# Kernel tuning notes

Measured on AMD Instinct MI355X. Metric: run time of the kernel, lower is better.

The kernel has to match this reference:

```python
import jax, jax.numpy as jnp
import numpy as np

EMBED, HEAD, CTX = 1024, 64, 2048

def setup_inputs() -> dict:
    key = jax.random.key(0)
    k1, k2, k3, k4 = jax.random.split(key, 4)
    x = jax.random.normal(k1, (16, 2048, EMBED), dtype=jnp.float32)
    s = EMBED ** -0.5  # torch Linear default init scale-ish
    Wq = jax.random.normal(k2, (EMBED, HEAD), dtype=jnp.float32) * s
    Wk = jax.random.normal(k3, (EMBED, HEAD), dtype=jnp.float32) * s
    Wv = jax.random.normal(k4, (EMBED, HEAD), dtype=jnp.float32) * s
    return {"x": x, "Wq": Wq, "Wk": Wk, "Wv": Wv}

def reference(x, Wq, Wk, Wv):
    # x: [B, S, E] -> q,k,v: [B, S, H]
    q = jnp.einsum('bse,eh->bsh', x, Wq)
    k = jnp.einsum('bse,eh->bsh', x, Wk)
    v = jnp.einsum('bse,eh->bsh', x, Wv)
    scale = k.shape[-1] ** -0.5
    scores = jnp.einsum('bqh,bkh->bqk', q, k) * scale  # [B, S, S]
    S = x.shape[1]
    causal = jnp.tril(jnp.ones((S, S), dtype=bool))
    scores = jnp.where(causal, scores, -jnp.inf)
    attn = jax.nn.softmax(scores, axis=-1)
    return jnp.einsum('bqk,bkh->bqh', attn, v)  # [B, S, H]
```

## Files before the change

### kernel.cpp

```cpp
#include <hip/hip_runtime.h>
#include <math.h>

#define BATCH 16
#define SEQ   2048
#define EMB   1024
#define HD    64
#define NROWS (BATCH*SEQ)

typedef __attribute__((ext_vector_type(8))) short short8;
typedef __attribute__((ext_vector_type(4))) float f32x4;

#define SWZ(byte, row) ((byte) ^ (((row) & 7) << 4))

__device__ __forceinline__ ushort f2bf(float f) {
    union { float f; unsigned u; } c; c.f = f;
    return (ushort)((c.u + 0x7FFF + ((c.u >> 16) & 1)) >> 16);
}

__global__ void k_transpose_w(const float* __restrict__ Wq,
                              const float* __restrict__ Wk,
                              const float* __restrict__ Wv,
                              ushort* __restrict__ wt) {
    int idx  = blockIdx.x * 256 + threadIdx.x;
    int c192 = idx >> 10;
    int e    = idx & 1023;
    const float* W = (c192 < 64) ? Wq : (c192 < 128 ? Wk : Wv);
    wt[idx] = f2bf(W[e * HD + (c192 & 63)]);
}

__global__ __launch_bounds__(256)
void k_qkv_proj(const float* __restrict__ x, const ushort* __restrict__ wt,
                ushort* __restrict__ qkv) {
    __shared__ short8 smem[(8192 + 24576) / 16];
    char* xls = (char*)smem;
    char* wls = (char*)smem + 8192;
    const int t = threadIdx.x;
    const int lane = t & 63, w = t >> 6;
    const int l15 = lane & 15, lg = lane >> 4;
    const int row0 = blockIdx.x * 64;

    f32x4 acc[3][4];
    #pragma unroll
    for (int mi = 0; mi < 3; ++mi)
        #pragma unroll
        for (int n = 0; n < 4; ++n) acc[mi][n] = (f32x4){0.f,0.f,0.f,0.f};

    for (int ch = 0; ch < EMB / 64; ++ch) {
        __syncthreads();
        #pragma unroll
        for (int i = 0; i < 4; ++i) {
            int c = t + i * 256;
            int r = c >> 4, f4 = c & 15;
            float4 v = *(const float4*)&x[(size_t)(row0 + r) * EMB + ch * 64 + f4 * 4];
            ushort4 bv;
            bv.x = f2bf(v.x); bv.y = f2bf(v.y); bv.z = f2bf(v.z); bv.w = f2bf(v.w);
            *(ushort4*)(xls + SWZ(r * 128 + f4 * 8, r)) = bv;
        }
        #pragma unroll
        for (int i = 0; i < 6; ++i) {
            int c = t + i * 256;
            int cr = c >> 3, j = c & 7;
            short8 v = *(const short8*)&wt[(size_t)cr * EMB + ch * 64 + j * 8];
            *(short8*)(wls + SWZ(cr * 128 + j * 16, cr)) = v;
        }
        __syncthreads();
        #pragma unroll
        for (int s = 0; s < 2; ++s) {
            short8 xf[4], wf[3];
            #pragma unroll
            for (int n = 0; n < 4; ++n) {
                int r = n * 16 + l15;
                xf[n] = *(short8*)(xls + SWZ(r * 128 + s * 64 + lg * 16, r));
            }
            #pragma unroll
            for (int mi = 0; mi < 3; ++mi) {
                int cr = w * 48 + mi * 16 + l15;
                wf[mi] = *(short8*)(wls + SWZ(cr * 128 + s * 64 + lg * 16, cr));
            }
            #pragma unroll
            for (int mi = 0; mi < 3; ++mi)
                #pragma unroll
                for (int n = 0; n < 4; ++n)
                    acc[mi][n] = __builtin_amdgcn_mfma_f32_16x16x32_bf16(
                        wf[mi], xf[n], acc[mi][n], 0, 0, 0);
        }
    }
    #pragma unroll
    for (int mi = 0; mi < 3; ++mi) {
        int cg0 = w * 48 + mi * 16 + 4 * lg;
        int m = cg0 >> 6, c = cg0 & 63;
        float sc = (m == 0) ? 0.125f : 1.0f;
        #pragma unroll
        for (int n = 0; n < 4; ++n) {
            int row = row0 + n * 16 + l15;
            ushort4 o;
            o.x = f2bf(acc[mi][n][0] * sc);
            o.y = f2bf(acc[mi][n][1] * sc);
            o.z = f2bf(acc[mi][n][2] * sc);
            o.w = f2bf(acc[mi][n][3] * sc);
            *(ushort4*)&qkv[((size_t)m * NROWS + row) * HD + c] = o;
        }
    }
}

__global__ __launch_bounds__(256)
void k_vt(const ushort* __restrict__ v, ushort* __restrict__ vt) {
    __shared__ short8 sm[64 * 72 / 8];
    ushort* lds = (ushort*)sm;
    const int t = threadIdx.x;
    const int b = blockIdx.x >> 5, k0 = (blockIdx.x & 31) * 64;
    #pragma unroll
    for (int i = 0; i < 2; ++i) {
        int c = t + i * 256;
        int key = c >> 3, j = c & 7;
        short8 d = *(const short8*)&v[((size_t)b * SEQ + k0 + key) * HD + j * 8];
        #pragma unroll
        for (int e = 0; e < 8; ++e) lds[(j * 8 + e) * 72 + key] = (ushort)d[e];
    }
    __syncthreads();
    #pragma unroll
    for (int i = 0; i < 2; ++i) {
        int c = t + i * 256;
        int hd = c >> 3, j = c & 7;
        short8 d = *(short8*)&lds[hd * 72 + j * 8];
        *(short8*)&vt[((size_t)b * HD + hd) * SEQ + k0 + j * 8] = d;
    }
}

__global__ __launch_bounds__(256)
void k_attn(const ushort* __restrict__ q, const ushort* __restrict__ k,
            const ushort* __restrict__ vt, float* __restrict__ out) {
    __shared__ short8 smem[(8192 + 8192 + 8192) / 16];
    char* kls = (char*)smem;
    char* vls = (char*)smem + 8192;
    char* pls = (char*)smem + 16384;
    const int t = threadIdx.x, lane = t & 63, w = t >> 6;
    const int l15 = lane & 15, lg = lane >> 4;
    const int b = blockIdx.x & 15, qt = 31 - (blockIdx.x >> 4);
    const int row0 = qt * 64;
    const int r0w = row0 + w * 16;
    const ushort* qb = q  + (size_t)b * SEQ * HD;
    const ushort* kb = k  + (size_t)b * SEQ * HD;
    const ushort* vb = vt + (size_t)b * HD * SEQ;
    char* pw = pls + w * 2048;

    short8 qf[2];
    #pragma unroll
    for (int s = 0; s < 2; ++s)
        qf[s] = *(const short8*)&qb[(size_t)(r0w + l15) * HD + s * 32 + lg * 8];

    f32x4 oacc[4];
    #pragma unroll
    for (int h = 0; h < 4; ++h) oacc[h] = (f32x4){0.f,0.f,0.f,0.f};
    float m_ = -INFINITY, l_ = 0.f;

    const int nkt = qt + 1;
    for (int kt = 0; kt < nkt; ++kt) {
        const int k0 = kt * 64;
        __syncthreads();
        #pragma unroll
        for (int i = 0; i < 2; ++i) {
            int c = t + i * 256;
            int r = c >> 3, j = c & 7;
            short8 kv = *(const short8*)&kb[(size_t)(k0 + r) * HD + j * 8];
            *(short8*)(kls + SWZ(r * 128 + j * 16, r)) = kv;
            short8 vv = *(const short8*)&vb[(size_t)r * SEQ + k0 + j * 8];
            *(short8*)(vls + SWZ(r * 128 + j * 16, r)) = vv;
        }
        __syncthreads();

        f32x4 sa[4];
        #pragma unroll
        for (int a = 0; a < 4; ++a) sa[a] = (f32x4){0.f,0.f,0.f,0.f};
        #pragma unroll
        for (int s = 0; s < 2; ++s)
            #pragma unroll
            for (int a = 0; a < 4; ++a) {
                int r = a * 16 + l15;
                short8 kf = *(short8*)(kls + SWZ(r * 128 + s * 64 + lg * 16, r));
                sa[a] = __builtin_amdgcn_mfma_f32_16x16x32_bf16(kf, qf[s], sa[a], 0, 0, 0);
            }

        if (kt == nkt - 1) {
            int qrow = r0w + l15;
            #pragma unroll
            for (int a = 0; a < 4; ++a)
                #pragma unroll
                for (int r = 0; r < 4; ++r)
                    if (k0 + a * 16 + 4 * lg + r > qrow) sa[a][r] = -INFINITY;
        }

        float smax = -INFINITY;
        #pragma unroll
        for (int a = 0; a < 4; ++a)
            #pragma unroll
            for (int r = 0; r < 4; ++r) smax = fmaxf(smax, sa[a][r]);
        smax = fmaxf(smax, __shfl_xor(smax, 16));
        smax = fmaxf(smax, __shfl_xor(smax, 32));
        float mn   = fmaxf(m_, smax);
        float corr = __expf(m_ - mn);
        float p[16], ps = 0.f;
        #pragma unroll
        for (int a = 0; a < 4; ++a)
            #pragma unroll
            for (int r = 0; r < 4; ++r) {
                float pv = __expf(sa[a][r] - mn);
                p[a * 4 + r] = pv; ps += pv;
            }
        ps += __shfl_xor(ps, 16);
        ps += __shfl_xor(ps, 32);
        l_ = l_ * corr + ps;
        m_ = mn;
        #pragma unroll
        for (int h = 0; h < 4; ++h) oacc[h] *= corr;

        #pragma unroll
        for (int a = 0; a < 4; ++a) {
            ushort4 pb;
            pb.x = f2bf(p[a * 4 + 0]); pb.y = f2bf(p[a * 4 + 1]);
            pb.z = f2bf(p[a * 4 + 2]); pb.w = f2bf(p[a * 4 + 3]);
            *(ushort4*)(pw + SWZ(l15 * 128 + a * 32 + lg * 8, l15)) = pb;
        }

        #pragma unroll
        for (int c = 0; c < 2; ++c) {
            short8 pf = *(short8*)(pw + SWZ(l15 * 128 + c * 64 + lg * 16, l15));
            #pragma unroll
            for (int h = 0; h < 4; ++h) {
                int r = h * 16 + l15;
                short8 vf = *(short8*)(vls + SWZ(r * 128 + c * 64 + lg * 16, r));
                oacc[h] = __builtin_amdgcn_mfma_f32_16x16x32_bf16(vf, pf, oacc[h], 0, 0, 0);
            }
        }
    }

    float inv = 1.0f / l_;
    #pragma unroll
    for (int h = 0; h < 4; ++h)
        #pragma unroll
        for (int r = 0; r < 4; ++r) {
            int hd = h * 16 + 4 * lg + r;
            out[((size_t)b * SEQ + r0w + l15) * HD + hd] = oacc[h][r] * inv;
        }
}

extern "C" void kernel_launch(void* const* d_in, const int* in_sizes, int n_in,
                              void* d_out, int out_size, void* d_ws, size_t ws_size,
                              hipStream_t stream) {
    const float* x  = (const float*)d_in[0];
    const float* Wq = (const float*)d_in[1];
    const float* Wk = (const float*)d_in[2];
    const float* Wv = (const float*)d_in[3];
    float* out = (float*)d_out;
    ushort* ws = (ushort*)d_ws;
    ushort* wt16  = ws;
    ushort* qkv16 = ws + 192 * 1024;
    ushort* vt16  = qkv16 + (size_t)3 * NROWS * HD;

    k_transpose_w<<<768, 256, 0, stream>>>(Wq, Wk, Wv, wt16);
    k_qkv_proj  <<<NROWS / 64, 256, 0, stream>>>(x, wt16, qkv16);
    k_vt        <<<BATCH * (SEQ / 64), 256, 0, stream>>>(
                    qkv16 + (size_t)2 * NROWS * HD, vt16);
    k_attn      <<<BATCH * (SEQ / 64), 256, 0, stream>>>(
                    qkv16, qkv16 + (size_t)NROWS * HD, vt16, out);
}
```

Measured before the change: 80.55 us.

## Double-buffer projection and attention loads, fuse V transpose, add lazy softmax rescale

```diff
diff --git a/kernel.cpp b/kernel.cpp
--- a/kernel.cpp
+++ b/kernel.cpp
@@ -10,11 +10,18 @@
 typedef __attribute__((ext_vector_type(8))) short short8;
 typedef __attribute__((ext_vector_type(4))) float f32x4;
 
-#define SWZ(byte, row) ((byte) ^ (((row) & 7) << 4))
+#define SWZ(byte, row)   ((byte) ^ (((row) & 7) << 4))
+#define SWZ16(byte, row) ((byte) ^ (((row) & 15) << 4))
 
 __device__ __forceinline__ ushort f2bf(float f) {
     union { float f; unsigned u; } c; c.f = f;
     return (ushort)((c.u + 0x7FFF + ((c.u >> 16) & 1)) >> 16);
+}
+
+__device__ __forceinline__ void gload_lds16(const void* g, void* l) {
+    __builtin_amdgcn_global_load_lds(
+        (const __attribute__((address_space(1))) void*)g,
+        (__attribute__((address_space(3))) void*)l, 16, 0, 0);
 }
 
 __global__ void k_transpose_w(const float* __restrict__ Wq,
@@ -30,12 +37,10 @@
 
 __global__ __launch_bounds__(256)
 void k_qkv_proj(const float* __restrict__ x, const ushort* __restrict__ wt,
-                ushort* __restrict__ qkv) {
-    __shared__ short8 smem[(8192 + 24576) / 16];
-    char* xls = (char*)smem;
-    char* wls = (char*)smem + 8192;
-    const int t = threadIdx.x;
-    const int lane = t & 63, w = t >> 6;
+                ushort* __restrict__ qkv, ushort* __restrict__ vt) {
+    __shared__ short8 smem[65536 / 16];
+    char* base = (char*)smem;
+    const int t = threadIdx.x, lane = t & 63, w = t >> 6;
     const int l15 = lane & 15, lg = lane >> 4;
     const int row0 = blockIdx.x * 64;
 
@@ -43,102 +48,137 @@
     #pragma unroll
     for (int mi = 0; mi < 3; ++mi)
         #pragma unroll
-        for (int n = 0; n < 4; ++n) acc[mi][n] = (f32x4){0.f,0.f,0.f,0.f};
-
-    for (int ch = 0; ch < EMB / 64; ++ch) {
-        __syncthreads();
-        #pragma unroll
-        for (int i = 0; i < 4; ++i) {
-            int c = t + i * 256;
-            int r = c >> 4, f4 = c & 15;
-            float4 v = *(const float4*)&x[(size_t)(row0 + r) * EMB + ch * 64 + f4 * 4];
-            ushort4 bv;
-            bv.x = f2bf(v.x); bv.y = f2bf(v.y); bv.z = f2bf(v.z); bv.w = f2bf(v.w);
-            *(ushort4*)(xls + SWZ(r * 128 + f4 * 8, r)) = bv;
-        }
+        for (int n = 0; n < 4; ++n) acc[mi][n] = (f32x4){0.f, 0.f, 0.f, 0.f};
+
+    float4 xr[2][2];
+
+    auto issue_x = [&](int ch) {
+        #pragma unroll
+        for (int i = 0; i < 2; ++i) {
+            int fidx = t + i * 256;
+            int r = fidx >> 3, j = fidx & 7;
+            const float* src = &x[(size_t)(row0 + r) * EMB + ch * 64 + j * 8];
+            xr[i][0] = *(const float4*)(src);
+            xr[i][1] = *(const float4*)(src + 4);
+        }
+    };
+    auto write_x = [&](int buf) {
+        char* xb = base + buf * 32768;
+        #pragma unroll
+        for (int i = 0; i < 2; ++i) {
+            int fidx = t + i * 256;
+            int r = fidx >> 3, j = fidx & 7;
+            short8 o;
+            o[0] = (short)f2bf(xr[i][0].x); o[1] = (short)f2bf(xr[i][0].y);
+            o[2] = (short)f2bf(xr[i][0].z); o[3] = (short)f2bf(xr[i][0].w);
+            o[4] = (short)f2bf(xr[i][1].x); o[5] = (short)f2bf(xr[i][1].y);
+            o[6] = (short)f2bf(xr[i][1].z); o[7] = (short)f2bf(xr[i][1].w);
+            *(short8*)(xb + SWZ(r * 128 + j * 16, r)) = o;
+        }
+    };
+    auto issue_w = [&](int ch, int buf) {
+        char* wb = base + buf * 32768 + 8192;
         #pragma unroll
         for (int i = 0; i < 6; ++i) {
-            int c = t + i * 256;
-            int cr = c >> 3, j = c & 7;
-            short8 v = *(const short8*)&wt[(size_t)cr * EMB + ch * 64 + j * 8];
-            *(short8*)(wls + SWZ(cr * 128 + j * 16, cr)) = v;
-        }
-        __syncthreads();
+            int r = (w * 6 + i) * 8 + (lane >> 3);
+            int j = (lane & 7) ^ (r & 7);
+            gload_lds16(&wt[(size_t)r * EMB + ch * 64 + j * 8],
+                        wb + (w * 6 + i) * 1024);
+        }
+    };
+    auto compute = [&](int buf) {
+        char* xb = base + buf * 32768;
+        char* wb = base + buf * 32768 + 8192;
         #pragma unroll
         for (int s = 0; s < 2; ++s) {
             short8 xf[4], wf[3];
             #pragma unroll
             for (int n = 0; n < 4; ++n) {
                 int r = n * 16 + l15;
-                xf[n] = *(short8*)(xls + SWZ(r * 128 + s * 64 + lg * 16, r));
+                xf[n] = *(short8*)(xb + SWZ(r * 128 + s * 64 + lg * 16, r));
             }
             #pragma unroll
             for (int mi = 0; mi < 3; ++mi) {
                 int cr = w * 48 + mi * 16 + l15;
-                wf[mi] = *(short8*)(wls + SWZ(cr * 128 + s * 64 + lg * 16, cr));
-            }
-            #pragma unroll
-            for (int mi = 0; mi < 3; ++mi)
+                wf[mi] = *(short8*)(wb + SWZ(cr * 128 + s * 64 + lg * 16, cr));
+            }
+            __builtin_amdgcn_s_setprio(1);
+            #pragma unroll
+            for (int mi = 0; mi < 3; ++mi) {
+                bool vsec = (w * 48 + mi * 16) >= 128;
                 #pragma unroll
                 for (int n = 0; n < 4; ++n)
-                    acc[mi][n] = __builtin_amdgcn_mfma_f32_16x16x32_bf16(
-                        wf[mi], xf[n], acc[mi][n], 0, 0, 0);
-        }
-    }
+                    acc[mi][n] = vsec
+                        ? __builtin_amdgcn_mfma_f32_16x16x32_bf16(xf[n], wf[mi], acc[mi][n], 0, 0, 0)
+                        : __builtin_amdgcn_mfma_f32_16x16x32_bf16(wf[mi], xf[n], acc[mi][n], 0, 0, 0);
+            }
+            __builtin_amdgcn_s_setprio(0);
+        }
+    };
+
+    issue_x(0); issue_w(0, 0); write_x(0);
+    __syncthreads();
+    for (int ch = 0; ch < 16; ++ch) {
+        int cur = ch & 1, nxt = cur ^ 1;
+        if (ch < 15) { issue_w(ch + 1, nxt); issue_x(ch + 1); }
+        compute(cur);
+        if (ch < 15) write_x(nxt);
+        __syncthreads();
+    }
+
+    char* qkb = base;
+    char* vtb = base + 16384;
+    const float qscale = 0.125f * 1.44269504f;
     #pragma unroll
     for (int mi = 0; mi < 3; ++mi) {
-        int cg0 = w * 48 + mi * 16 + 4 * lg;
-        int m = cg0 >> 6, c = cg0 & 63;
-        float sc = (m == 0) ? 0.125f : 1.0f;
+        int cg0 = w * 48 + mi * 16;
+        bool vsec = cg0 >= 128;
         #pragma unroll
         for (int n = 0; n < 4; ++n) {
-            int row = row0 + n * 16 + l15;
             ushort4 o;
-            o.x = f2bf(acc[mi][n][0] * sc);
-            o.y = f2bf(acc[mi][n][1] * sc);
-            o.z = f2bf(acc[mi][n][2] * sc);
-            o.w = f2bf(acc[mi][n][3] * sc);
-            *(ushort4*)&qkv[((size_t)m * NROWS + row) * HD + c] = o;
-        }
-    }
-}
-
-__global__ __launch_bounds__(256)
-void k_vt(const ushort* __restrict__ v, ushort* __restrict__ vt) {
-    __shared__ short8 sm[64 * 72 / 8];
-    ushort* lds = (ushort*)sm;
-    const int t = threadIdx.x;
-    const int b = blockIdx.x >> 5, k0 = (blockIdx.x & 31) * 64;
+            if (!vsec) {
+                float sc = (cg0 < 64) ? qscale : 1.0f;
+                o.x = f2bf(acc[mi][n][0] * sc); o.y = f2bf(acc[mi][n][1] * sc);
+                o.z = f2bf(acc[mi][n][2] * sc); o.w = f2bf(acc[mi][n][3] * sc);
+                int xrow = n * 16 + l15, c = cg0 + lg * 4;
+                *(ushort4*)(qkb + SWZ16(xrow * 256 + c * 2, xrow)) = o;
+            } else {
+                o.x = f2bf(acc[mi][n][0]); o.y = f2bf(acc[mi][n][1]);
+                o.z = f2bf(acc[mi][n][2]); o.w = f2bf(acc[mi][n][3]);
+                int hd = cg0 - 128 + l15, key = n * 16 + lg * 4;
+                *(ushort4*)(vtb + SWZ(hd * 128 + key * 2, hd)) = o;
+            }
+        }
+    }
+    __syncthreads();
+    const int b = row0 >> 11, r0b = row0 & 2047;
+    #pragma unroll
+    for (int i = 0; i < 4; ++i) {
+        int idx = t + i * 256;
+        int r = idx >> 4, g = idx & 15;
+        short8 v = *(short8*)(qkb + SWZ16(r * 256 + g * 16, r));
+        int c0 = g * 8, m = c0 >> 6, c = c0 & 63;
+        *(short8*)&qkv[((size_t)m * NROWS + row0 + r) * HD + c] = v;
+    }
     #pragma unroll
     for (int i = 0; i < 2; ++i) {
-        int c = t + i * 256;
-        int key = c >> 3, j = c & 7;
-        short8 d = *(const short8*)&v[((size_t)b * SEQ + k0 + key) * HD + j * 8];
-        #pragma unroll
-        for (int e = 0; e < 8; ++e) lds[(j * 8 + e) * 72 + key] = (ushort)d[e];
-    }
-    __syncthreads();
-    #pragma unroll
-    for (int i = 0; i < 2; ++i) {
-        int c = t + i * 256;
-        int hd = c >> 3, j = c & 7;
-        short8 d = *(short8*)&lds[hd * 72 + j * 8];
-        *(short8*)&vt[((size_t)b * HD + hd) * SEQ + k0 + j * 8] = d;
+        int idx = t + i * 256;
+        int hd = idx >> 3, g = idx & 7;
+        short8 v = *(short8*)(vtb + SWZ(hd * 128 + g * 16, hd));
+        *(short8*)&vt[((size_t)b * HD + hd) * SEQ + r0b + g * 8] = v;
     }
 }
 
 __global__ __launch_bounds__(256)
 void k_attn(const ushort* __restrict__ q, const ushort* __restrict__ k,
             const ushort* __restrict__ vt, float* __restrict__ out) {
-    __shared__ short8 smem[(8192 + 8192 + 8192) / 16];
-    char* kls = (char*)smem;
-    char* vls = (char*)smem + 8192;
-    char* pls = (char*)smem + 16384;
+    __shared__ short8 smem[40960 / 16];
+    char* base = (char*)smem;
+    char* pls  = base + 32768;
     const int t = threadIdx.x, lane = t & 63, w = t >> 6;
     const int l15 = lane & 15, lg = lane >> 4;
     const int b = blockIdx.x & 15, qt = 31 - (blockIdx.x >> 4);
-    const int row0 = qt * 64;
-    const int r0w = row0 + w * 16;
+    const int row0 = qt * 64, r0w = row0 + w * 16;
     const ushort* qb = q  + (size_t)b * SEQ * HD;
     const ushort* kb = k  + (size_t)b * SEQ * HD;
     const ushort* vb = vt + (size_t)b * HD * SEQ;
@@ -151,27 +191,36 @@
 
     f32x4 oacc[4];
     #pragma unroll
-    for (int h = 0; h < 4; ++h) oacc[h] = (f32x4){0.f,0.f,0.f,0.f};
+    for (int h = 0; h < 4; ++h) oacc[h] = (f32x4){0.f, 0.f, 0.f, 0.f};
     float m_ = -INFINITY, l_ = 0.f;
 
+    auto stage = [&](int kt, int buf) {
+        char* kbuf = base + buf * 16384;
+        char* vbuf = kbuf + 8192;
+        int k0 = kt * 64;
+        #pragma unroll
+        for (int i = 0; i < 2; ++i) {
+            int r = (w * 2 + i) * 8 + (lane >> 3);
+            int j = (lane & 7) ^ (r & 7);
+            gload_lds16(&kb[(size_t)(k0 + r) * HD + j * 8], kbuf + (w * 2 + i) * 1024);
+            gload_lds16(&vb[(size_t)r * SEQ + k0 + j * 8],  vbuf + (w * 2 + i) * 1024);
+        }
+    };
+
     const int nkt = qt + 1;
+    stage(0, 0);
+    __syncthreads();
     for (int kt = 0; kt < nkt; ++kt) {
-        const int k0 = kt * 64;
-        __syncthreads();
-        #pragma unroll
-        for (int i = 0; i < 2; ++i) {
-            int c = t + i * 256;
-            int r = c >> 3, j = c & 7;
-            short8 kv = *(const short8*)&kb[(size_t)(k0 + r) * HD + j * 8];
-            *(short8*)(kls + SWZ(r * 128 + j * 16, r)) = kv;
-            short8 vv = *(const short8*)&vb[(size_t)r * SEQ + k0 + j * 8];
-            *(short8*)(vls + SWZ(r * 128 + j * 16, r)) = vv;
-        }
-        __syncthreads();
+        int cur = kt & 1;
+        if (kt + 1 < nkt) stage(kt + 1, cur ^ 1);
+        char* kls = base + cur * 16384;
+        char* vls = kls + 8192;
+        int k0 = kt * 64;
 
         f32x4 sa[4];
         #pragma unroll
-        for (int a = 0; a < 4; ++a) sa[a] = (f32x4){0.f,0.f,0.f,0.f};
+        for (int a = 0; a < 4; ++a) sa[a] = (f32x4){0.f, 0.f, 0.f, 0.f};
+        __builtin_amdgcn_s_setprio(1);
         #pragma unroll
         for (int s = 0; s < 2; ++s)
             #pragma unroll
@@ -180,6 +229,7 @@
                 short8 kf = *(short8*)(kls + SWZ(r * 128 + s * 64 + lg * 16, r));
                 sa[a] = __builtin_amdgcn_mfma_f32_16x16x32_bf16(kf, qf[s], sa[a], 0, 0, 0);
             }
+        __builtin_amdgcn_s_setprio(0);
 
         if (kt == nkt - 1) {
             int qrow = r0w + l15;
@@ -187,7 +237,7 @@
             for (int a = 0; a < 4; ++a)
                 #pragma unroll
                 for (int r = 0; r < 4; ++r)
-                    if (k0 + a * 16 + 4 * lg + r > qrow) sa[a][r] = -INFINITY;
+                    if (k0 + a * 16 + lg * 4 + r > qrow) sa[a][r] = -INFINITY;
         }
 
         float smax = -INFINITY;
@@ -197,22 +247,25 @@
             for (int r = 0; r < 4; ++r) smax = fmaxf(smax, sa[a][r]);
         smax = fmaxf(smax, __shfl_xor(smax, 16));
         smax = fmaxf(smax, __shfl_xor(smax, 32));
-        float mn   = fmaxf(m_, smax);
-        float corr = __expf(m_ - mn);
+        if (!__all(smax - m_ <= 8.0f)) {
+            float mn   = fmaxf(m_, smax);
+            float corr = __builtin_amdgcn_exp2f(m_ - mn);
+            l_ *= corr;
+            #pragma unroll
+            for (int h = 0; h < 4; ++h) oacc[h] *= corr;
+            m_ = mn;
+        }
         float p[16], ps = 0.f;
         #pragma unroll
         for (int a = 0; a < 4; ++a)
             #pragma unroll
             for (int r = 0; r < 4; ++r) {
-                float pv = __expf(sa[a][r] - mn);
+                float pv = __builtin_amdgcn_exp2f(sa[a][r] - m_);
                 p[a * 4 + r] = pv; ps += pv;
             }
         ps += __shfl_xor(ps, 16);
         ps += __shfl_xor(ps, 32);
-        l_ = l_ * corr + ps;
-        m_ = mn;
-        #pragma unroll
-        for (int h = 0; h < 4; ++h) oacc[h] *= corr;
+        l_ += ps;
 
         #pragma unroll
         for (int a = 0; a < 4; ++a) {
@@ -222,6 +275,7 @@
             *(ushort4*)(pw + SWZ(l15 * 128 + a * 32 + lg * 8, l15)) = pb;
         }
 
+        __builtin_amdgcn_s_setprio(1);
         #pragma unroll
         for (int c = 0; c < 2; ++c) {
             short8 pf = *(short8*)(pw + SWZ(l15 * 128 + c * 64 + lg * 16, l15));
@@ -232,16 +286,25 @@
                 oacc[h] = __builtin_amdgcn_mfma_f32_16x16x32_bf16(vf, pf, oacc[h], 0, 0, 0);
             }
         }
+        __builtin_amdgcn_s_setprio(0);
+        __syncthreads();
     }
 
     float inv = 1.0f / l_;
     #pragma unroll
-    for (int h = 0; h < 4; ++h)
-        #pragma unroll
-        for (int r = 0; r < 4; ++r) {
-            int hd = h * 16 + 4 * lg + r;
-            out[((size_t)b * SEQ + r0w + l15) * HD + hd] = oacc[h][r] * inv;
-        }
+    for (int h = 0; h < 4; ++h) {
+        f32x4 v = oacc[h] * inv;
+        int qr = w * 16 + l15;
+        *(f32x4*)(base + SWZ16(qr * 256 + h * 64 + lg * 16, qr)) = v;
+    }
+    __syncthreads();
+    #pragma unroll
+    for (int i = 0; i < 4; ++i) {
+        int idx = t + i * 256;
+        int r = idx >> 4, g = idx & 15;
+        f32x4 v = *(f32x4*)(base + SWZ16(r * 256 + g * 16, r));
+        *(f32x4*)&out[((size_t)b * SEQ + row0 + r) * HD + g * 4] = v;
+    }
 }
 
 extern "C" void kernel_launch(void* const* d_in, const int* in_sizes, int n_in,
@@ -253,14 +316,12 @@
     const float* Wv = (const float*)d_in[3];
     float* out = (float*)d_out;
     ushort* ws = (ushort*)d_ws;
-    ushort* wt16  = ws;
-    ushort* qkv16 = ws + 192 * 1024;
-    ushort* vt16  = qkv16 + (size_t)3 * NROWS * HD;
+    ushort* wt16 = ws;
+    ushort* qk16 = ws + 192 * 1024;
+    ushort* vt16 = qk16 + (size_t)2 * NROWS * HD;
 
     k_transpose_w<<<768, 256, 0, stream>>>(Wq, Wk, Wv, wt16);
-    k_qkv_proj  <<<NROWS / 64, 256, 0, stream>>>(x, wt16, qkv16);
-    k_vt        <<<BATCH * (SEQ / 64), 256, 0, stream>>>(
-                    qkv16 + (size_t)2 * NROWS * HD, vt16);
+    k_qkv_proj  <<<NROWS / 64, 256, 0, stream>>>(x, wt16, qk16, vt16);
     k_attn      <<<BATCH * (SEQ / 64), 256, 0, stream>>>(
-                    qkv16, qkv16 + (size_t)NROWS * HD, vt16, out);
-}
+                    qk16, qk16 + (size_t)NROWS * HD, vt16, out);
+}
```

Result: faster. 72.34 us (-10.2%).
